# Kernel tuning notes

Measured on AMD Instinct MI355X. Metric: run time of the kernel, lower is better.

Reference implementation:

```python
import jax, jax.numpy as jnp
import numpy as np

N = 50000
E = 800000
D_IN = 128
D_HID = 128
D_OUT = 64
BN_EPS = 1e-5


def setup_inputs() -> dict:
    key = jax.random.key(0)
    ks = jax.random.split(key, 8)
    x = jax.random.normal(ks[0], (N, D_IN), dtype=jnp.float32)
    edge_index = jax.random.randint(ks[1], (2, E), 0, N, dtype=jnp.int64)
    # fc1
    W1 = jax.random.normal(ks[2], (D_IN, D_HID), dtype=jnp.float32) / np.sqrt(D_IN)
    b1 = jnp.zeros((D_HID,), dtype=jnp.float32)
    # bn1 affine params
    gamma = jnp.ones((D_HID,), dtype=jnp.float32)
    beta = jnp.zeros((D_HID,), dtype=jnp.float32)
    # fc2
    W2 = jax.random.normal(ks[3], (D_HID, D_OUT), dtype=jnp.float32) / np.sqrt(D_HID)
    b2 = jnp.zeros((D_OUT,), dtype=jnp.float32)
    return {"x": x, "W1": W1, "b1": b1, "gamma": gamma, "beta": beta,
            "W2": W2, "b2": b2, "edge_index": edge_index}


def _propagate(x, row, col):
    # add self loops for every node (reference convention)
    n = x.shape[0]
    sl = jnp.arange(n, dtype=row.dtype)
    row_f = jnp.concatenate([row, sl])
    col_f = jnp.concatenate([col, sl])
    # symmetric degree normalization: deg computed over destinations (col)
    deg = jax.ops.segment_sum(jnp.ones_like(col_f, dtype=x.dtype), col_f, num_segments=n)
    dis = deg ** -0.5
    w = dis[col_f] * dis[row_f]                       # [E+N]
    msg = w[:, None] * x[row_f]                       # [E+N, D] gather + scale
    return jax.ops.segment_sum(msg, col_f, num_segments=n)  # scatter-add


def reference(x, W1, b1, gamma, beta, W2, b2, edge_index):
    row, col = edge_index[0], edge_index[1]
    h = x @ W1 + b1                                   # [N, D_HID]
    h = _propagate(h, row, col)
    # BatchNorm1d with batch statistics (training-mode math, deterministic)
    mu = jnp.mean(h, axis=0)
    var = jnp.var(h, axis=0)
    h = (h - mu) * jax.lax.rsqrt(var + BN_EPS) * gamma + beta
    h = jax.nn.relu(h)
    # dropout treated as identity (eval) for a deterministic reference
    h = h @ W2 + b2                                   # [N, D_OUT]
    h = _propagate(h, row, col)
    return jax.nn.log_softmax(h, axis=1)
```

## Files before the change

### kernel.cpp

```cpp
#include <hip/hip_runtime.h>
#include <hip/hip_bf16.h>

#define N_NODES 50000
#define NE      800000
#define DIN     128
#define DHID    128
#define DOUT    64
#define BN_EPS  1e-5f
#define SLOT    64
#define NBUK    98
#define BCAP    8704
#define EPB     2048
#define LDW     132
#define LDW2    132

typedef __hip_bfloat16 bf16;
typedef short bf16x8 __attribute__((ext_vector_type(8)));
typedef float f32x4 __attribute__((ext_vector_type(4)));

__device__ __forceinline__ float ldf(const void* p, int i, int isbf) {
    if (isbf) return __bfloat162float(((const bf16*)p)[i]);
    return ((const float*)p)[i];
}
__device__ __forceinline__ unsigned short f2b(float f) {
    bf16 h = __float2bfloat16(f);
    return *(unsigned short*)&h;
}
__device__ __forceinline__ float2 up2(unsigned int u) {
    return make_float2(__uint_as_float(u << 16), __uint_as_float(u & 0xffff0000u));
}
__device__ __forceinline__ unsigned int pk2(float a, float b) {
    return ((unsigned int)f2b(a)) | (((unsigned int)f2b(b)) << 16);
}

#define DETECT_ISBF(W1raw, tid, sdet, isbf_out)                                   \
    if ((tid) == 0) sdet = 0;                                                     \
    __syncthreads();                                                              \
    {                                                                             \
        unsigned int u_ = ((unsigned int)((const unsigned short*)(W1raw))[tid]) << 16; \
        float f_ = fabsf(__uint_as_float(u_));                                    \
        if (!isnan(f_) && !isinf(f_) && f_ > 1e4f) atomicOr(&sdet, 1);            \
    }                                                                             \
    __syncthreads();                                                              \
    const int isbf_out = !sdet;

__global__ __launch_bounds__(256) void k_binA(const void* eiraw, int* __restrict__ gcnt,
                                              int* __restrict__ counts, unsigned int* __restrict__ bpk) {
    __shared__ int hist[128], lofs[128], cur[128], gbase[128];
    __shared__ unsigned int stg[EPB];
    __shared__ int sdet;
    int tid = threadIdx.x;
    for (int i = blockIdx.x * 256 + tid; i < N_NODES; i += gridDim.x * 256) counts[i] = 0;
    if (tid == 0) sdet = 0;
    if (tid < 128) hist[tid] = 0;
    __syncthreads();
    if (tid < 64 && ((const unsigned int*)eiraw)[2 * tid + 1] != 0u) atomicOr(&sdet, 1);
    __syncthreads();
    const int isll = !sdet;

    int e0 = blockIdx.x * EPB;
    int nE = NE - e0; if (nE > EPB) nE = EPB;
    int r[8], c[8];
    #pragma unroll
    for (int q = 0; q < 8; ++q) {
        int li = q * 256 + tid;
        if (li < nE) {
            int e = e0 + li;
            if (isll) { r[q] = (int)((const long long*)eiraw)[e]; c[q] = (int)((const long long*)eiraw)[NE + e]; }
            else      { r[q] = ((const int*)eiraw)[e];            c[q] = ((const int*)eiraw)[NE + e]; }
            atomicAdd(&hist[c[q] >> 9], 1);
        } else r[q] = -1;
    }
    __syncthreads();
    if (tid == 0) {
        int acc = 0;
        for (int b = 0; b < NBUK; ++b) { lofs[b] = acc; acc += hist[b]; }
    }
    __syncthreads();
    if (tid < NBUK) { gbase[tid] = atomicAdd(&gcnt[tid], hist[tid]); cur[tid] = lofs[tid]; }
    __syncthreads();
    #pragma unroll
    for (int q = 0; q < 8; ++q) {
        if (r[q] >= 0) {
            int b = c[q] >> 9;
            int p = atomicAdd(&cur[b], 1);
            stg[p] = ((unsigned int)b << 25) | ((unsigned int)(c[q] & 511) << 16) | (unsigned int)r[q];
        }
    }
    __syncthreads();
    for (int i = tid; i < nE; i += 256) {
        unsigned int v = stg[i];
        int b = v >> 25;
        int pos = gbase[b] + (i - lofs[b]);
        if (pos < BCAP) bpk[b * BCAP + pos] = v;
    }
}

__global__ __launch_bounds__(256) void k_binB(const unsigned int* __restrict__ bpk, const int* __restrict__ gcnt,
                                              int* __restrict__ counts, int* __restrict__ ej) {
    int b = blockIdx.x >> 2;
    int part = blockIdx.x & 3;
    int m = gcnt[b]; if (m > BCAP) m = BCAP;
    const unsigned int* src = bpk + b * BCAP;
    for (int i = part * 256 + threadIdx.x; i < m; i += 1024) {
        unsigned int v = src[i];
        int c = (b << 9) | ((v >> 16) & 511);
        int s = v & 0xffff;
        int k = atomicAdd(&counts[c], 1);
        if (k < SLOT) ej[c * SLOT + k] = s;
    }
}

__global__ __launch_bounds__(256) void k_gemm1_mfma(const void* __restrict__ x, const void* __restrict__ W1,
                                                    const void* __restrict__ b1, const int* __restrict__ counts,
                                                    unsigned short* __restrict__ g1) {
    __shared__ unsigned short wt[128 * LDW];
    __shared__ int sdet;
    int tid = threadIdx.x;
    DETECT_ISBF(W1, tid, sdet, isbf)

    #pragma unroll 4
    for (int i = 0; i < 64; ++i) {
        int idx = i * 256 + tid;
        int k = idx >> 7, n = idx & 127;
        wt[n * LDW + k] = isbf ? ((const unsigned short*)W1)[idx]
                               : f2b(((const float*)W1)[idx]);
    }
    __syncthreads();

    int lane = tid & 63;
    int wave = tid >> 6;
    int m0 = blockIdx.x * 64 + wave * 16;
    int lm = lane & 15;
    int quad = lane >> 4;

    bf16x8 a[4];
    int arow = m0 + lm;
    int arow_c = arow < N_NODES ? arow : 0;
    if (isbf) {
        const unsigned short* xb = (const unsigned short*)x;
        #pragma unroll
        for (int q = 0; q < 4; ++q)
            a[q] = *(const bf16x8*)(xb + arow_c * DIN + q * 32 + quad * 8);
    } else {
        const float* xf = (const float*)x;
        #pragma unroll
        for (int q = 0; q < 4; ++q) {
            bf16x8 t;
            #pragma unroll
            for (int j = 0; j < 8; ++j)
                t[j] = (short)f2b(xf[arow_c * DIN + q * 32 + quad * 8 + j]);
            a[q] = t;
        }
    }

    float dsc[4];
    #pragma unroll
    for (int r = 0; r < 4; ++r) {
        int grow = m0 + quad * 4 + r;
        dsc[r] = (grow < N_NODES) ? rsqrtf((float)(counts[grow] + 1)) : 0.f;
    }

    #pragma unroll
    for (int nt = 0; nt < 8; ++nt) {
        int n0 = nt * 16;
        f32x4 acc = {0.f, 0.f, 0.f, 0.f};
        #pragma unroll
        for (int q = 0; q < 4; ++q) {
            bf16x8 b = *(const bf16x8*)(wt + (n0 + lm) * LDW + q * 32 + quad * 8);
            acc = __builtin_amdgcn_mfma_f32_16x16x32_bf16(a[q], b, acc, 0, 0, 0);
        }
        float bias = ldf(b1, n0 + lm, isbf);
        #pragma unroll
        for (int r = 0; r < 4; ++r) {
            int grow = m0 + quad * 4 + r;
            if (grow < N_NODES)
                g1[grow * DHID + n0 + lm] = f2b(dsc[r] * (acc[r] + bias));
        }
    }
}

__global__ __launch_bounds__(256) void k_prop1(const int* __restrict__ counts, const int* __restrict__ ej,
                                               const unsigned int* __restrict__ g1p,
                                               unsigned int* __restrict__ agg1p) {
    int tid = threadIdx.x;
    int n = blockIdx.x * 4 + (tid >> 6);
    n = __builtin_amdgcn_readfirstlane(n);
    if (n >= N_NODES) return;
    int lane = tid & 63;
    int cnt = counts[n];
    int t = cnt < SLOT ? cnt : SLOT;
    const int* ejn = ej + (size_t)n * SLOT;
    float2 v = up2(g1p[(size_t)n * 64 + lane]);
    float ax0 = v.x, ay0 = v.y, ax1 = 0.f, ay1 = 0.f;
    float ax2 = 0.f, ay2 = 0.f, ax3 = 0.f, ay3 = 0.f;
    int j = 0;
    for (; j + 8 <= t; j += 8) {
        int e0 = ejn[j], e1 = ejn[j + 1], e2 = ejn[j + 2], e3 = ejn[j + 3];
        int e4 = ejn[j + 4], e5 = ejn[j + 5], e6 = ejn[j + 6], e7 = ejn[j + 7];
        unsigned int g0 = g1p[(size_t)e0 * 64 + lane];
        unsigned int g1_ = g1p[(size_t)e1 * 64 + lane];
        unsigned int g2 = g1p[(size_t)e2 * 64 + lane];
        unsigned int g3 = g1p[(size_t)e3 * 64 + lane];
        unsigned int g4 = g1p[(size_t)e4 * 64 + lane];
        unsigned int g5 = g1p[(size_t)e5 * 64 + lane];
        unsigned int g6 = g1p[(size_t)e6 * 64 + lane];
        unsigned int g7 = g1p[(size_t)e7 * 64 + lane];
        float2 f0 = up2(g0), f1 = up2(g1_), f2 = up2(g2), f3 = up2(g3);
        float2 f4 = up2(g4), f5 = up2(g5), f6 = up2(g6), f7 = up2(g7);
        ax0 += f0.x; ay0 += f0.y; ax1 += f1.x; ay1 += f1.y;
        ax2 += f2.x; ay2 += f2.y; ax3 += f3.x; ay3 += f3.y;
        ax0 += f4.x; ay0 += f4.y; ax1 += f5.x; ay1 += f5.y;
        ax2 += f6.x; ay2 += f6.y; ax3 += f7.x; ay3 += f7.y;
    }
    for (; j < t; ++j) {
        float2 f = up2(g1p[(size_t)ejn[j] * 64 + lane]);
        ax0 += f.x; ay0 += f.y;
    }
    float dv = rsqrtf((float)(cnt + 1));
    float ax = dv * ((ax0 + ax1) + (ax2 + ax3));
    float ay = dv * ((ay0 + ay1) + (ay2 + ay3));
    agg1p[(size_t)n * 64 + lane] = pk2(ax, ay);
}

__global__ __launch_bounds__(256) void k_stats(const unsigned int* __restrict__ agg1p, float* __restrict__ stats) {
    int tid = threadIdx.x;
    const int total = N_NODES * 64;
    float sx = 0.f, sy = 0.f, qx = 0.f, qy = 0.f;
    for (int idx = blockIdx.x * 256 + tid; idx < total; idx += gridDim.x * 256) {
        float2 v = up2(agg1p[idx]);
        sx += v.x; sy += v.y; qx += v.x * v.x; qy += v.y * v.y;
    }
    __shared__ float lsx[256], lsy[256], lqx[256], lqy[256];
    lsx[tid] = sx; lsy[tid] = sy; lqx[tid] = qx; lqy[tid] = qy;
    __syncthreads();
    if (tid < 64) {
        float tsx = lsx[tid] + lsx[tid + 64] + lsx[tid + 128] + lsx[tid + 192];
        float tsy = lsy[tid] + lsy[tid + 64] + lsy[tid + 128] + lsy[tid + 192];
        float tqx = lqx[tid] + lqx[tid + 64] + lqx[tid + 128] + lqx[tid + 192];
        float tqy = lqy[tid] + lqy[tid + 64] + lqy[tid + 128] + lqy[tid + 192];
        atomicAdd(&stats[2 * tid], tsx);
        atomicAdd(&stats[2 * tid + 1], tsy);
        atomicAdd(&stats[128 + 2 * tid], tqx);
        atomicAdd(&stats[128 + 2 * tid + 1], tqy);
    }
}

__global__ __launch_bounds__(256) void k_gemm2_mfma(const unsigned int* __restrict__ agg1p,
                                                    const float* __restrict__ stats,
                                                    const void* __restrict__ gamma, const void* __restrict__ beta,
                                                    const void* __restrict__ W2, const void* __restrict__ b2,
                                                    const void* __restrict__ W1, const int* __restrict__ counts,
                                                    unsigned short* __restrict__ g2) {
    __shared__ unsigned short w2t[64 * LDW2];
    __shared__ float sc[128], sh[128];
    __shared__ int sdet;
    int tid = threadIdx.x;
    DETECT_ISBF(W1, tid, sdet, isbf)

    #pragma unroll 4
    for (int i = 0; i < 32; ++i) {
        int idx = i * 256 + tid;
        int k = idx >> 6, n = idx & 63;
        w2t[n * LDW2 + k] = isbf ? ((const unsigned short*)W2)[idx]
                                 : f2b(((const float*)W2)[idx]);
    }
    if (tid < 128) {
        const float invn = 1.0f / (float)N_NODES;
        float mu = stats[tid] * invn;
        float var = stats[128 + tid] * invn - mu * mu;
        float rs = rsqrtf(var + BN_EPS);
        float g = ldf(gamma, tid, isbf);
        sc[tid] = rs * g;
        sh[tid] = ldf(beta, tid, isbf) - mu * rs * g;
    }
    __syncthreads();

    int lane = tid & 63;
    int wave = tid >> 6;
    int m0 = blockIdx.x * 64 + wave * 16;
    int lm = lane & 15;
    int quad = lane >> 4;

    int arow = m0 + lm;
    int arow_c = arow < N_NODES ? arow : 0;
    bf16x8 a[4];
    #pragma unroll
    for (int q = 0; q < 4; ++q) {
        uint4 gv = *(const uint4*)(agg1p + (size_t)arow_c * 64 + q * 16 + quad * 4);
        int kb = q * 32 + quad * 8;
        float2 f0 = up2(gv.x), f1 = up2(gv.y), f2 = up2(gv.z), f3 = up2(gv.w);
        float e0 = f0.x * sc[kb + 0] + sh[kb + 0];
        float e1 = f0.y * sc[kb + 1] + sh[kb + 1];
        float e2 = f1.x * sc[kb + 2] + sh[kb + 2];
        float e3 = f1.y * sc[kb + 3] + sh[kb + 3];
        float e4 = f2.x * sc[kb + 4] + sh[kb + 4];
        float e5 = f2.y * sc[kb + 5] + sh[kb + 5];
        float e6 = f3.x * sc[kb + 6] + sh[kb + 6];
        float e7 = f3.y * sc[kb + 7] + sh[kb + 7];
        bf16x8 t;
        t[0] = (short)f2b(e0 > 0.f ? e0 : 0.f);
        t[1] = (short)f2b(e1 > 0.f ? e1 : 0.f);
        t[2] = (short)f2b(e2 > 0.f ? e2 : 0.f);
        t[3] = (short)f2b(e3 > 0.f ? e3 : 0.f);
        t[4] = (short)f2b(e4 > 0.f ? e4 : 0.f);
        t[5] = (short)f2b(e5 > 0.f ? e5 : 0.f);
        t[6] = (short)f2b(e6 > 0.f ? e6 : 0.f);
        t[7] = (short)f2b(e7 > 0.f ? e7 : 0.f);
        a[q] = t;
    }

    float dsc[4];
    #pragma unroll
    for (int r = 0; r < 4; ++r) {
        int grow = m0 + quad * 4 + r;
        dsc[r] = (grow < N_NODES) ? rsqrtf((float)(counts[grow] + 1)) : 0.f;
    }

    #pragma unroll
    for (int nt = 0; nt < 4; ++nt) {
        int n0 = nt * 16;
        f32x4 acc = {0.f, 0.f, 0.f, 0.f};
        #pragma unroll
        for (int q = 0; q < 4; ++q) {
            bf16x8 b = *(const bf16x8*)(w2t + (n0 + lm) * LDW2 + q * 32 + quad * 8);
            acc = __builtin_amdgcn_mfma_f32_16x16x32_bf16(a[q], b, acc, 0, 0, 0);
        }
        float bias = ldf(b2, n0 + lm, isbf);
        #pragma unroll
        for (int r = 0; r < 4; ++r) {
            int grow = m0 + quad * 4 + r;
            if (grow < N_NODES)
                g2[grow * DOUT + n0 + lm] = f2b(dsc[r] * (acc[r] + bias));
        }
    }
}

__global__ __launch_bounds__(256) void k_prop2_lsm(const int* __restrict__ counts, const int* __restrict__ ej,
                                                   const unsigned int* __restrict__ g2p,
                                                   const void* __restrict__ W1, void* __restrict__ out) {
    __shared__ int sdet;
    int tid = threadIdx.x;
    DETECT_ISBF(W1, tid, sdet, isbf)

    int n = blockIdx.x * 8 + (tid >> 5);
    if (n >= N_NODES) return;
    int lane = tid & 31;
    int cnt = counts[n];
    int t = cnt < SLOT ? cnt : SLOT;
    const int* ejn = ej + (size_t)n * SLOT;
    float2 v = up2(g2p[(size_t)n * 32 + lane]);
    float ax0 = v.x, ay0 = v.y, ax1 = 0.f, ay1 = 0.f;
    float ax2 = 0.f, ay2 = 0.f, ax3 = 0.f, ay3 = 0.f;
    int j = 0;
    for (; j + 16 <= t; j += 16) {
        int e[16]; unsigned int gg[16];
        #pragma unroll
        for (int q = 0; q < 16; ++q) e[q] = ejn[j + q];
        #pragma unroll
        for (int q = 0; q < 16; ++q) gg[q] = g2p[(size_t)e[q] * 32 + lane];
        #pragma unroll
        for (int q = 0; q < 16; ++q) {
            float2 f = up2(gg[q]);
            if ((q & 3) == 0) { ax0 += f.x; ay0 += f.y; }
            else if ((q & 3) == 1) { ax1 += f.x; ay1 += f.y; }
            else if ((q & 3) == 2) { ax2 += f.x; ay2 += f.y; }
            else { ax3 += f.x; ay3 += f.y; }
        }
    }
    for (; j + 4 <= t; j += 4) {
        int e0 = ejn[j], e1 = ejn[j + 1], e2 = ejn[j + 2], e3 = ejn[j + 3];
        unsigned int g0 = g2p[(size_t)e0 * 32 + lane];
        unsigned int g1_ = g2p[(size_t)e1 * 32 + lane];
        unsigned int g2 = g2p[(size_t)e2 * 32 + lane];
        unsigned int g3 = g2p[(size_t)e3 * 32 + lane];
        float2 f0 = up2(g0), f1 = up2(g1_), f2 = up2(g2), f3 = up2(g3);
        ax0 += f0.x; ay0 += f0.y; ax1 += f1.x; ay1 += f1.y;
        ax2 += f2.x; ay2 += f2.y; ax3 += f3.x; ay3 += f3.y;
    }
    for (; j < t; ++j) {
        float2 f = up2(g2p[(size_t)ejn[j] * 32 + lane]);
        ax0 += f.x; ay0 += f.y;
    }
    float dv = rsqrtf((float)(cnt + 1));
    float ax = dv * ((ax0 + ax1) + (ax2 + ax3));
    float ay = dv * ((ay0 + ay1) + (ay2 + ay3));
    float m = fmaxf(ax, ay);
    #pragma unroll
    for (int off = 16; off >= 1; off >>= 1) m = fmaxf(m, __shfl_xor(m, off, 32));
    float sum = __expf(ax - m) + __expf(ay - m);
    #pragma unroll
    for (int off = 16; off >= 1; off >>= 1) sum += __shfl_xor(sum, off, 32);
    float lse = m + __logf(sum);
    float rx = ax - lse, ry = ay - lse;
    if (isbf) {
        ((unsigned int*)out)[(size_t)n * 32 + lane] = pk2(rx, ry);
    } else {
        float2* o = (float2*)((float*)out + (size_t)n * 64 + 2 * lane);
        *o = make_float2(rx, ry);
    }
}

extern "C" void kernel_launch(void* const* d_in, const int* in_sizes, int n_in,
                              void* d_out, int out_size, void* d_ws, size_t ws_size,
                              hipStream_t stream) {
    const void* x     = d_in[0];
    const void* W1    = d_in[1];
    const void* b1    = d_in[2];
    const void* gamma = d_in[3];
    const void* beta  = d_in[4];
    const void* W2    = d_in[5];
    const void* b2    = d_in[6];
    const void* ei    = d_in[7];

    char* w = (char*)d_ws;
    float*          stats  = (float*)(w + 0);
    int*            gcnt   = (int*)(w + 1024);
    int*            counts = (int*)(w + 2048);
    int*            ej     = (int*)(w + 202048);
    unsigned int*   bpk    = (unsigned int*)(w + 13002048);
    unsigned short* g1     = (unsigned short*)(w + 16414016);
    unsigned int*   agg1p  = (unsigned int*)(w + 29214016);
    unsigned short* g2     = (unsigned short*)(w + 42014016);

    hipMemsetAsync(w, 0, 2048, stream);

    k_binA<<<(NE + EPB - 1) / EPB, 256, 0, stream>>>(ei, gcnt, counts, bpk);
    k_binB<<<NBUK * 4, 256, 0, stream>>>(bpk, gcnt, counts, ej);

    k_gemm1_mfma<<<(N_NODES + 63) / 64, 256, 0, stream>>>(x, W1, b1, counts, g1);

    k_prop1<<<(N_NODES + 3) / 4, 256, 0, stream>>>(counts, ej, (const unsigned int*)g1, agg1p);

    k_stats<<<256, 256, 0, stream>>>((const unsigned int*)agg1p, stats);

    k_gemm2_mfma<<<(N_NODES + 63) / 64, 256, 0, stream>>>(agg1p, stats, gamma, beta, W2, b2,
                                                          W1, counts, g2);

    k_prop2_lsm<<<(N_NODES + 7) / 8, 256, 0, stream>>>(counts, ej, (const unsigned int*)g2, W1, d_out);
}
```

Measured before the change: 254.9 us.

## Counting-sort edges in LDS per bucket and fuse BN stats into propagation

Binning now uses 196 buckets of 256 destination nodes. The second pass does a shared-memory counting sort per bucket, so it writes counts and ej directly without global atomics on counts and without zeroing counts. The separate BN statistics kernel is removed: k_prop1 reduces the sum and sum of squares per block and atomically adds them into 32 partial stat slices, which gemm2 then sums. This cuts a kernel launch and a full re-read of agg1, and removes global atomic contention, at the cost of more shared memory in binB and fewer, larger binB blocks.

```diff
diff --git a/kernel.cpp b/kernel.cpp
--- a/kernel.cpp
+++ b/kernel.cpp
@@ -8,9 +8,10 @@
 #define DOUT    64
 #define BN_EPS  1e-5f
 #define SLOT    64
-#define NBUK    98
-#define BCAP    8704
+#define NBUK    196
+#define BCAP    4864
 #define EPB     2048
+#define NPART   32
 #define LDW     132
 #define LDW2    132
 
@@ -45,14 +46,13 @@
     const int isbf_out = !sdet;
 
 __global__ __launch_bounds__(256) void k_binA(const void* eiraw, int* __restrict__ gcnt,
-                                              int* __restrict__ counts, unsigned int* __restrict__ bpk) {
-    __shared__ int hist[128], lofs[128], cur[128], gbase[128];
+                                              unsigned int* __restrict__ bpk) {
+    __shared__ int hist[256], scanb[256], eofs[256], cur[256], gbase[256];
     __shared__ unsigned int stg[EPB];
     __shared__ int sdet;
     int tid = threadIdx.x;
-    for (int i = blockIdx.x * 256 + tid; i < N_NODES; i += gridDim.x * 256) counts[i] = 0;
     if (tid == 0) sdet = 0;
-    if (tid < 128) hist[tid] = 0;
+    hist[tid] = 0;
     __syncthreads();
     if (tid < 64 && ((const unsigned int*)eiraw)[2 * tid + 1] != 0u) atomicOr(&sdet, 1);
     __syncthreads();
@@ -68,46 +68,82 @@
             int e = e0 + li;
             if (isll) { r[q] = (int)((const long long*)eiraw)[e]; c[q] = (int)((const long long*)eiraw)[NE + e]; }
             else      { r[q] = ((const int*)eiraw)[e];            c[q] = ((const int*)eiraw)[NE + e]; }
-            atomicAdd(&hist[c[q] >> 9], 1);
+            atomicAdd(&hist[c[q] >> 8], 1);
         } else r[q] = -1;
     }
     __syncthreads();
-    if (tid == 0) {
-        int acc = 0;
-        for (int b = 0; b < NBUK; ++b) { lofs[b] = acc; acc += hist[b]; }
-    }
-    __syncthreads();
-    if (tid < NBUK) { gbase[tid] = atomicAdd(&gcnt[tid], hist[tid]); cur[tid] = lofs[tid]; }
+    int hv = hist[tid];
+    scanb[tid] = hv;
+    __syncthreads();
+    for (int off = 1; off < 256; off <<= 1) {
+        int u = (tid >= off) ? scanb[tid - off] : 0;
+        __syncthreads();
+        scanb[tid] += u;
+        __syncthreads();
+    }
+    int ex = scanb[tid] - hv;
+    eofs[tid] = ex;
+    cur[tid] = ex;
+    if (tid < NBUK) gbase[tid] = atomicAdd(&gcnt[tid], hv);
     __syncthreads();
     #pragma unroll
     for (int q = 0; q < 8; ++q) {
         if (r[q] >= 0) {
-            int b = c[q] >> 9;
+            int b = c[q] >> 8;
             int p = atomicAdd(&cur[b], 1);
-            stg[p] = ((unsigned int)b << 25) | ((unsigned int)(c[q] & 511) << 16) | (unsigned int)r[q];
+            stg[p] = ((unsigned int)b << 24) | ((unsigned int)(c[q] & 255) << 16) | (unsigned int)r[q];
         }
     }
     __syncthreads();
     for (int i = tid; i < nE; i += 256) {
         unsigned int v = stg[i];
-        int b = v >> 25;
-        int pos = gbase[b] + (i - lofs[b]);
-        if (pos < BCAP) bpk[b * BCAP + pos] = v;
+        int b = v >> 24;
+        int pos = gbase[b] + (i - eofs[b]);
+        if (pos < BCAP) bpk[(size_t)b * BCAP + pos] = v;
     }
 }
 
 __global__ __launch_bounds__(256) void k_binB(const unsigned int* __restrict__ bpk, const int* __restrict__ gcnt,
                                               int* __restrict__ counts, int* __restrict__ ej) {
-    int b = blockIdx.x >> 2;
-    int part = blockIdx.x & 3;
+    __shared__ int cnt[256], scanb[256], eofs[256], cur[256];
+    __shared__ unsigned int stg[BCAP];
+    int b = blockIdx.x;
+    int tid = threadIdx.x;
     int m = gcnt[b]; if (m > BCAP) m = BCAP;
-    const unsigned int* src = bpk + b * BCAP;
-    for (int i = part * 256 + threadIdx.x; i < m; i += 1024) {
+    cnt[tid] = 0;
+    __syncthreads();
+    const unsigned int* src = bpk + (size_t)b * BCAP;
+    for (int i = tid; i < m; i += 256)
+        atomicAdd(&cnt[(src[i] >> 16) & 255], 1);
+    __syncthreads();
+    int hv = cnt[tid];
+    scanb[tid] = hv;
+    __syncthreads();
+    for (int off = 1; off < 256; off <<= 1) {
+        int u = (tid >= off) ? scanb[tid - off] : 0;
+        __syncthreads();
+        scanb[tid] += u;
+        __syncthreads();
+    }
+    int ex = scanb[tid] - hv;
+    eofs[tid] = ex;
+    cur[tid] = ex;
+    __syncthreads();
+    for (int i = tid; i < m; i += 256) {
         unsigned int v = src[i];
-        int c = (b << 9) | ((v >> 16) & 511);
-        int s = v & 0xffff;
-        int k = atomicAdd(&counts[c], 1);
-        if (k < SLOT) ej[c * SLOT + k] = s;
+        int cl = (v >> 16) & 255;
+        int p = atomicAdd(&cur[cl], 1);
+        stg[p] = v & 0x00ffffffu;
+    }
+    __syncthreads();
+    int c0 = b << 8;
+    int cg = c0 + tid;
+    if (cg < N_NODES) counts[cg] = hv;
+    for (int i = tid; i < m; i += 256) {
+        unsigned int v = stg[i];
+        int cl = v >> 16;
+        int k = i - eofs[cl];
+        if (k < SLOT) ej[(size_t)(c0 + cl) * SLOT + k] = (int)(v & 0xffffu);
     }
 }
 
@@ -182,78 +218,67 @@
 
 __global__ __launch_bounds__(256) void k_prop1(const int* __restrict__ counts, const int* __restrict__ ej,
                                                const unsigned int* __restrict__ g1p,
-                                               unsigned int* __restrict__ agg1p) {
-    int tid = threadIdx.x;
-    int n = blockIdx.x * 4 + (tid >> 6);
+                                               unsigned int* __restrict__ agg1p,
+                                               float* __restrict__ statsP) {
+    __shared__ float sp[1024];
+    int tid = threadIdx.x;
+    int w = tid >> 6;
+    int n = blockIdx.x * 4 + w;
     n = __builtin_amdgcn_readfirstlane(n);
-    if (n >= N_NODES) return;
     int lane = tid & 63;
-    int cnt = counts[n];
-    int t = cnt < SLOT ? cnt : SLOT;
-    const int* ejn = ej + (size_t)n * SLOT;
-    float2 v = up2(g1p[(size_t)n * 64 + lane]);
-    float ax0 = v.x, ay0 = v.y, ax1 = 0.f, ay1 = 0.f;
-    float ax2 = 0.f, ay2 = 0.f, ax3 = 0.f, ay3 = 0.f;
-    int j = 0;
-    for (; j + 8 <= t; j += 8) {
-        int e0 = ejn[j], e1 = ejn[j + 1], e2 = ejn[j + 2], e3 = ejn[j + 3];
-        int e4 = ejn[j + 4], e5 = ejn[j + 5], e6 = ejn[j + 6], e7 = ejn[j + 7];
-        unsigned int g0 = g1p[(size_t)e0 * 64 + lane];
-        unsigned int g1_ = g1p[(size_t)e1 * 64 + lane];
-        unsigned int g2 = g1p[(size_t)e2 * 64 + lane];
-        unsigned int g3 = g1p[(size_t)e3 * 64 + lane];
-        unsigned int g4 = g1p[(size_t)e4 * 64 + lane];
-        unsigned int g5 = g1p[(size_t)e5 * 64 + lane];
-        unsigned int g6 = g1p[(size_t)e6 * 64 + lane];
-        unsigned int g7 = g1p[(size_t)e7 * 64 + lane];
-        float2 f0 = up2(g0), f1 = up2(g1_), f2 = up2(g2), f3 = up2(g3);
-        float2 f4 = up2(g4), f5 = up2(g5), f6 = up2(g6), f7 = up2(g7);
-        ax0 += f0.x; ay0 += f0.y; ax1 += f1.x; ay1 += f1.y;
-        ax2 += f2.x; ay2 += f2.y; ax3 += f3.x; ay3 += f3.y;
-        ax0 += f4.x; ay0 += f4.y; ax1 += f5.x; ay1 += f5.y;
-        ax2 += f6.x; ay2 += f6.y; ax3 += f7.x; ay3 += f7.y;
-    }
-    for (; j < t; ++j) {
-        float2 f = up2(g1p[(size_t)ejn[j] * 64 + lane]);
-        ax0 += f.x; ay0 += f.y;
-    }
-    float dv = rsqrtf((float)(cnt + 1));
-    float ax = dv * ((ax0 + ax1) + (ax2 + ax3));
-    float ay = dv * ((ay0 + ay1) + (ay2 + ay3));
-    agg1p[(size_t)n * 64 + lane] = pk2(ax, ay);
-}
-
-__global__ __launch_bounds__(256) void k_stats(const unsigned int* __restrict__ agg1p, float* __restrict__ stats) {
-    int tid = threadIdx.x;
-    const int total = N_NODES * 64;
-    float sx = 0.f, sy = 0.f, qx = 0.f, qy = 0.f;
-    for (int idx = blockIdx.x * 256 + tid; idx < total; idx += gridDim.x * 256) {
-        float2 v = up2(agg1p[idx]);
-        sx += v.x; sy += v.y; qx += v.x * v.x; qy += v.y * v.y;
-    }
-    __shared__ float lsx[256], lsy[256], lqx[256], lqy[256];
-    lsx[tid] = sx; lsy[tid] = sy; lqx[tid] = qx; lqy[tid] = qy;
-    __syncthreads();
-    if (tid < 64) {
-        float tsx = lsx[tid] + lsx[tid + 64] + lsx[tid + 128] + lsx[tid + 192];
-        float tsy = lsy[tid] + lsy[tid + 64] + lsy[tid + 128] + lsy[tid + 192];
-        float tqx = lqx[tid] + lqx[tid + 64] + lqx[tid + 128] + lqx[tid + 192];
-        float tqy = lqy[tid] + lqy[tid + 64] + lqy[tid + 128] + lqy[tid + 192];
-        atomicAdd(&stats[2 * tid], tsx);
-        atomicAdd(&stats[2 * tid + 1], tsy);
-        atomicAdd(&stats[128 + 2 * tid], tqx);
-        atomicAdd(&stats[128 + 2 * tid + 1], tqy);
-    }
+    float ax = 0.f, ay = 0.f;
+    if (n < N_NODES) {
+        int cnt = counts[n];
+        int t = cnt < SLOT ? cnt : SLOT;
+        const int* ejn = ej + (size_t)n * SLOT;
+        float2 v = up2(g1p[(size_t)n * 64 + lane]);
+        float ax0 = v.x, ay0 = v.y, ax1 = 0.f, ay1 = 0.f;
+        float ax2 = 0.f, ay2 = 0.f, ax3 = 0.f, ay3 = 0.f;
+        int j = 0;
+        for (; j + 8 <= t; j += 8) {
+            int e0 = ejn[j], e1 = ejn[j + 1], e2 = ejn[j + 2], e3 = ejn[j + 3];
+            int e4 = ejn[j + 4], e5 = ejn[j + 5], e6 = ejn[j + 6], e7 = ejn[j + 7];
+            unsigned int g0 = g1p[(size_t)e0 * 64 + lane];
+            unsigned int g1_ = g1p[(size_t)e1 * 64 + lane];
+            unsigned int g2 = g1p[(size_t)e2 * 64 + lane];
+            unsigned int g3 = g1p[(size_t)e3 * 64 + lane];
+            unsigned int g4 = g1p[(size_t)e4 * 64 + lane];
+            unsigned int g5 = g1p[(size_t)e5 * 64 + lane];
+            unsigned int g6 = g1p[(size_t)e6 * 64 + lane];
+            unsigned int g7 = g1p[(size_t)e7 * 64 + lane];
+            float2 f0 = up2(g0), f1 = up2(g1_), f2 = up2(g2), f3 = up2(g3);
+            float2 f4 = up2(g4), f5 = up2(g5), f6 = up2(g6), f7 = up2(g7);
+            ax0 += f0.x; ay0 += f0.y; ax1 += f1.x; ay1 += f1.y;
+            ax2 += f2.x; ay2 += f2.y; ax3 += f3.x; ay3 += f3.y;
+            ax0 += f4.x; ay0 += f4.y; ax1 += f5.x; ay1 += f5.y;
+            ax2 += f6.x; ay2 += f6.y; ax3 += f7.x; ay3 += f7.y;
+        }
+        for (; j < t; ++j) {
+            float2 f = up2(g1p[(size_t)ejn[j] * 64 + lane]);
+            ax0 += f.x; ay0 += f.y;
+        }
+        float dv = rsqrtf((float)(cnt + 1));
+        ax = dv * ((ax0 + ax1) + (ax2 + ax3));
+        ay = dv * ((ay0 + ay1) + (ay2 + ay3));
+        agg1p[(size_t)n * 64 + lane] = pk2(ax, ay);
+    }
+    sp[w * 256 + 2 * lane]       = ax;
+    sp[w * 256 + 2 * lane + 1]   = ay;
+    sp[w * 256 + 128 + 2 * lane] = ax * ax;
+    sp[w * 256 + 129 + 2 * lane] = ay * ay;
+    __syncthreads();
+    float s = sp[tid] + sp[256 + tid] + sp[512 + tid] + sp[768 + tid];
+    atomicAdd(&statsP[(blockIdx.x & (NPART - 1)) * 256 + tid], s);
 }
 
 __global__ __launch_bounds__(256) void k_gemm2_mfma(const unsigned int* __restrict__ agg1p,
-                                                    const float* __restrict__ stats,
+                                                    const float* __restrict__ statsP,
                                                     const void* __restrict__ gamma, const void* __restrict__ beta,
                                                     const void* __restrict__ W2, const void* __restrict__ b2,
                                                     const void* __restrict__ W1, const int* __restrict__ counts,
                                                     unsigned short* __restrict__ g2) {
     __shared__ unsigned short w2t[64 * LDW2];
-    __shared__ float sc[128], sh[128];
+    __shared__ float sc[128], sh[128], redu[256];
     __shared__ int sdet;
     int tid = threadIdx.x;
     DETECT_ISBF(W1, tid, sdet, isbf)
@@ -265,10 +290,17 @@
         w2t[n * LDW2 + k] = isbf ? ((const unsigned short*)W2)[idx]
                                  : f2b(((const float*)W2)[idx]);
     }
+    {
+        float s = 0.f;
+        #pragma unroll
+        for (int p = 0; p < NPART; ++p) s += statsP[p * 256 + tid];
+        redu[tid] = s;
+    }
+    __syncthreads();
     if (tid < 128) {
         const float invn = 1.0f / (float)N_NODES;
-        float mu = stats[tid] * invn;
-        float var = stats[128 + tid] * invn - mu * mu;
+        float mu = redu[tid] * invn;
+        float var = redu[128 + tid] * invn - mu * mu;
         float rs = rsqrtf(var + BN_EPS);
         float g = ldf(gamma, tid, isbf);
         sc[tid] = rs * g;
@@ -414,27 +446,25 @@
     const void* ei    = d_in[7];
 
     char* w = (char*)d_ws;
-    float*          stats  = (float*)(w + 0);
-    int*            gcnt   = (int*)(w + 1024);
-    int*            counts = (int*)(w + 2048);
-    int*            ej     = (int*)(w + 202048);
-    unsigned int*   bpk    = (unsigned int*)(w + 13002048);
-    unsigned short* g1     = (unsigned short*)(w + 16414016);
-    unsigned int*   agg1p  = (unsigned int*)(w + 29214016);
-    unsigned short* g2     = (unsigned short*)(w + 42014016);
-
-    hipMemsetAsync(w, 0, 2048, stream);
-
-    k_binA<<<(NE + EPB - 1) / EPB, 256, 0, stream>>>(ei, gcnt, counts, bpk);
-    k_binB<<<NBUK * 4, 256, 0, stream>>>(bpk, gcnt, counts, ej);
+    float*          statsP = (float*)(w + 0);
+    int*            gcnt   = (int*)(w + 32768);
+    int*            counts = (int*)(w + 33792);
+    int*            ej     = (int*)(w + 233792);
+    unsigned int*   bpk    = (unsigned int*)(w + 13033792);
+    unsigned short* g1     = (unsigned short*)(w + 16847168);
+    unsigned int*   agg1p  = (unsigned int*)(w + 29647168);
+    unsigned short* g2     = (unsigned short*)(w + 42447168);
+
+    hipMemsetAsync(w, 0, 33792, stream);
+
+    k_binA<<<(NE + EPB - 1) / EPB, 256, 0, stream>>>(ei, gcnt, bpk);
+    k_binB<<<NBUK, 256, 0, stream>>>(bpk, gcnt, counts, ej);
 
     k_gemm1_mfma<<<(N_NODES + 63) / 64, 256, 0, stream>>>(x, W1, b1, counts, g1);
 
-    k_prop1<<<(N_NODES + 3) / 4, 256, 0, stream>>>(counts, ej, (const unsigned int*)g1, agg1p);
-
-    k_stats<<<256, 256, 0, stream>>>((const unsigned int*)agg1p, stats);
-
-    k_gemm2_mfma<<<(N_NODES + 63) / 64, 256, 0, stream>>>(agg1p, stats, gamma, beta, W2, b2,
+    k_prop1<<<(N_NODES + 3) / 4, 256, 0, stream>>>(counts, ej, (const unsigned int*)g1, agg1p, statsP);
+
+    k_gemm2_mfma<<<(N_NODES + 63) / 64, 256, 0, stream>>>(agg1p, statsP, gamma, beta, W2, b2,
                                                           W1, counts, g2);
 
     k_prop2_lsm<<<(N_NODES + 7) / 8, 256, 0, stream>>>(counts, ej, (const unsigned int*)g2, W1, d_out);
```

Measured after the change: 226.6 us. 11.1% less time.
